# Kernel optimization log

Measured on AMD Instinct MI355X. Metric: run time of the kernel, lower is better.

Reference implementation:

```python
import jax, jax.numpy as jnp
import numpy as np
from jax.ops import segment_sum

N_NODES = 100000
IN, HID, OUT = 512, 128, 40
N_EDGES = 1600000


def gcn_conv(x, W, b, src, dst, n):
    # x: [N, d_in] -> linear transform first (PyG GCNConv applies lin before propagate)
    h = x @ W  # [N, d_out]
    # add self-loops
    loop = jnp.arange(n, dtype=src.dtype)
    s = jnp.concatenate([src, loop])
    d = jnp.concatenate([dst, loop])
    # symmetric normalization deg^{-1/2}[s] * deg^{-1/2}[d], deg over targets incl. self-loops
    deg = segment_sum(jnp.ones_like(d, dtype=h.dtype), d, num_segments=n)
    dinv = jnp.where(deg > 0, jax.lax.rsqrt(deg), 0.0)
    norm = dinv[s] * dinv[d]  # [E+N]
    msg = h[s] * norm[:, None]  # gather + scale
    out = segment_sum(msg, d, num_segments=n)  # scatter-add over edges
    return out + b


def setup_inputs() -> dict:
    key = jax.random.key(0)
    k1, k2, k3, k4, k5, k6 = jax.random.split(key, 6)
    x = jax.random.normal(k1, (N_NODES, IN), dtype=jnp.float32)
    edge_index = jax.random.randint(k2, (2, N_EDGES), 0, N_NODES, dtype=jnp.int64)
    s1 = 1.0 / np.sqrt(IN)
    s2 = 1.0 / np.sqrt(HID)
    W1 = jax.random.uniform(k3, (IN, HID), jnp.float32, -s1, s1)
    b1 = jnp.zeros((HID,), jnp.float32)
    W2 = jax.random.uniform(k4, (HID, OUT), jnp.float32, -s2, s2)
    b2 = jnp.zeros((OUT,), jnp.float32)
    return {"x": x, "edge_index": edge_index, "W1": W1, "b1": b1, "W2": W2, "b2": b2}


def reference(x, edge_index, W1, b1, W2, b2):
    src, dst = edge_index[0], edge_index[1]
    n = x.shape[0]
    # CRD: GCNConv -> relu (dropout is identity in eval mode)
    h = jax.nn.relu(gcn_conv(x, W1, b1, src, dst, n))
    # CLS: GCNConv -> log_softmax
    out = gcn_conv(h, W2, b2, src, dst, n)
    return jax.nn.log_softmax(out, axis=1)
```

## Files before the change

### kernel.cpp

```cpp
#include <hip/hip_runtime.h>
#include <hip/hip_bf16.h>

typedef unsigned short u16;
typedef __attribute__((ext_vector_type(8))) short short8;
typedef __attribute__((ext_vector_type(4))) float f32x4;

#define NN   100000
#define NE   1600000
#define DIN  512
#define DHID 128
#define DOUT 40
#define NB   98

__device__ __forceinline__ float bf2f(u16 u) {
  union { unsigned int i; float f; } v; v.i = ((unsigned int)u) << 16; return v.f;
}
__device__ __forceinline__ u16 f2bf(float f) {
  __hip_bfloat16 h = __float2bfloat16(f);
  return *reinterpret_cast<u16*>(&h);
}


__global__ __launch_bounds__(256) void k_count(const int* __restrict__ ei, int* __restrict__ cnt) {
  int base = (blockIdx.x * 256 + threadIdx.x) * 4;
  if (base >= NE) return;
  int4 d4 = *(const int4*)&ei[NE + base];
  atomicAdd(&cnt[d4.x], 1);
  atomicAdd(&cnt[d4.y], 1);
  atomicAdd(&cnt[d4.z], 1);
  atomicAdd(&cnt[d4.w], 1);
}

__global__ __launch_bounds__(256) void k_dinv(const int* __restrict__ cnt, float* __restrict__ dinv) {
  int i = blockIdx.x * 256 + threadIdx.x;
  if (i < NN) dinv[i] = rsqrtf((float)(cnt[i] + 1));
}

__global__ __launch_bounds__(256) void k_blocksum(const int* __restrict__ cnt, int* __restrict__ bsum) {
  __shared__ int s[256];
  int b = blockIdx.x, t = threadIdx.x;
  int base = b * 1024 + t * 4;
  int tot = 0;
  if (base < NN) { int4 v = *(const int4*)&cnt[base]; tot = v.x + v.y + v.z + v.w; }
  s[t] = tot; __syncthreads();
  for (int o = 128; o > 0; o >>= 1) { if (t < o) s[t] += s[t + o]; __syncthreads(); }
  if (t == 0) bsum[b] = s[0];
}

__global__ __launch_bounds__(128) void k_scanbsum(int* __restrict__ bsum) {
  __shared__ int s[128];
  int t = threadIdx.x;
  int v = (t < NB) ? bsum[t] : 0;
  s[t] = v; __syncthreads();
  for (int o = 1; o < 128; o <<= 1) {
    int add = (t >= o) ? s[t - o] : 0;
    __syncthreads();
    s[t] += add;
    __syncthreads();
  }
  if (t < NB) bsum[t] = s[t] - v;
}

__global__ __launch_bounds__(256) void k_scan3(const int* __restrict__ cnt, const int* __restrict__ bsum,
                                               int* __restrict__ offs, int* __restrict__ cur) {
  __shared__ int s[256];
  int b = blockIdx.x, t = threadIdx.x;
  int base = b * 1024 + t * 4;
  int4 v = make_int4(0, 0, 0, 0);
  if (base < NN) v = *(const int4*)&cnt[base];
  int tot = v.x + v.y + v.z + v.w;
  s[t] = tot; __syncthreads();
  for (int o = 1; o < 256; o <<= 1) {
    int add = (t >= o) ? s[t - o] : 0;
    __syncthreads();
    s[t] += add;
    __syncthreads();
  }
  int tp = s[t] - tot;
  int b0 = bsum[b] + tp;
  if (base < NN) {
    int4 o4;
    o4.x = b0;
    o4.y = b0 + v.x;
    o4.z = b0 + v.x + v.y;
    o4.w = b0 + v.x + v.y + v.z;
    *(int4*)&offs[base] = o4;
    *(int4*)&cur[base]  = o4;
  }
  if (b == 0 && t == 0) offs[NN] = NE;
}

__global__ __launch_bounds__(256) void k_scatter(const int* __restrict__ ei, int* __restrict__ cur,
                                                 const float* __restrict__ dinv, int2* __restrict__ ep) {
  int base = (blockIdx.x * 256 + threadIdx.x) * 4;
  if (base >= NE) return;
  int4 s4 = *(const int4*)&ei[base];
  int4 d4 = *(const int4*)&ei[NE + base];
  int p0 = atomicAdd(&cur[d4.x], 1);
  int p1 = atomicAdd(&cur[d4.y], 1);
  int p2 = atomicAdd(&cur[d4.z], 1);
  int p3 = atomicAdd(&cur[d4.w], 1);
  ep[p0] = make_int2(s4.x, __float_as_int(dinv[s4.x]));
  ep[p1] = make_int2(s4.y, __float_as_int(dinv[s4.y]));
  ep[p2] = make_int2(s4.z, __float_as_int(dinv[s4.z]));
  ep[p3] = make_int2(s4.w, __float_as_int(dinv[s4.w]));
}


__global__ __launch_bounds__(256) void k_prepw(const float* __restrict__ W1, u16* __restrict__ wt) {
  int id = blockIdx.x * 256 + threadIdx.x;
  int k = id & 511, n = id >> 9;
  wt[n * DIN + k] = f2bf(W1[k * DHID + n]);
}


#define G1_LOAD(S, C) do { int k0_ = (C) * 64;                                          \
  _Pragma("unroll") for (int it = 0; it < 4; it++) {                                    \
    int u_ = t + it * 256; int row_ = u_ >> 4, seg_ = u_ & 15; int gr_ = row0 + row_;   \
    xv[S][it] = (gr_ < NN) ? *(const float4*)&x[gr_ * DIN + k0_ + seg_ * 4]             \
                           : make_float4(0.f, 0.f, 0.f, 0.f);                           \
    wv[S][it] = *(const uint4*)&wt[(u_ >> 3) * DIN + k0_ + (u_ & 7) * 8];               \
  } } while (0)

#define G1_WRITE(S) do {                                                                \
  _Pragma("unroll") for (int it = 0; it < 4; it++) {                                    \
    int u_ = t + it * 256; int row_ = u_ >> 4, seg_ = u_ & 15;                          \
    float4 v_ = xv[S][it]; ushort4 o_;                                                  \
    o_.x = f2bf(v_.x); o_.y = f2bf(v_.y); o_.z = f2bf(v_.z); o_.w = f2bf(v_.w);         \
    *(ushort4*)&xs[S][row_][seg_ * 4] = o_;                                             \
    *(uint4*)&ws[S][u_ >> 3][(u_ & 7) * 8] = wv[S][it];                                 \
  } } while (0)

#define G1_MFMA(S) do {                                                                 \
  _Pragma("unroll") for (int s2 = 0; s2 < 2; s2++) {                                    \
    short8 a_ = *(const short8*)&xs[S][mbase + lm][s2 * 32 + lq * 8];                   \
    _Pragma("unroll") for (int nt = 0; nt < 8; nt++) {                                  \
      short8 b_ = *(const short8*)&ws[S][nt * 16 + lm][s2 * 32 + lq * 8];               \
      acc[nt] = __builtin_amdgcn_mfma_f32_16x16x32_bf16(a_, b_, acc[nt], 0, 0, 0);      \
    } } } while (0)

#define G1_BAR() do {                                                                   \
    asm volatile("s_waitcnt lgkmcnt(0)" ::: "memory");                                  \
    __builtin_amdgcn_sched_barrier(0);          \
    __builtin_amdgcn_s_barrier();                                                       \
  } while (0)

__global__ __launch_bounds__(256) void k_gemm1(const float* __restrict__ x, const u16* __restrict__ wt,
                                               u16* __restrict__ h1) {
  __shared__ u16 xs[2][64][72];
  __shared__ u16 ws[2][128][72];
  int t = threadIdx.x;
  int row0 = blockIdx.x * 64;
  int w = t >> 6, l = t & 63;
  int lm = l & 15, lq = l >> 4;
  int mbase = w * 16;
  float4 xv[2][4];
  uint4  wv[2][4];
  f32x4 acc[8];
#pragma unroll
  for (int nt = 0; nt < 8; nt++) acc[nt] = (f32x4){0.f, 0.f, 0.f, 0.f};

  G1_LOAD(0, 0);
  G1_LOAD(1, 1);
  G1_WRITE(0);
  G1_BAR();

#pragma unroll
  for (int c = 0; c < 8; c++) {
    if (c + 2 < 8) {
      if ((c & 1) == 0) G1_LOAD(0, c + 2); else G1_LOAD(1, c + 2);
    }
    if ((c & 1) == 0) G1_MFMA(0); else G1_MFMA(1);
    if (c + 1 < 8) {
      if ((c & 1) == 0) G1_WRITE(1); else G1_WRITE(0);
      G1_BAR();
    }
  }

#pragma unroll
  for (int reg = 0; reg < 4; reg++) {
    int gr = row0 + mbase + lq * 4 + reg;
    if (gr < NN) {
#pragma unroll
      for (int nt = 0; nt < 8; nt++) {
        h1[gr * DHID + nt * 16 + lm] = f2bf(acc[nt][reg]);
      }
    }
  }
}


__global__ __launch_bounds__(256) void k_prop1(const u16* __restrict__ h1, const float* __restrict__ dinv,
                                               const int* __restrict__ offs, const int2* __restrict__ ep,
                                               const float* __restrict__ b1, u16* __restrict__ g) {
  int n = blockIdx.x * 4 + (threadIdx.x >> 6);
  int l = threadIdx.x & 63;
  int qtr = l >> 4, c = l & 15;
  int fb = c * 8;
  float dn = dinv[n];
  float a[8];
#pragma unroll
  for (int j = 0; j < 8; j++) a[j] = 0.f;
  if (qtr == 0) {
    short8 sv = *(const short8*)&h1[n * DHID + fb];
#pragma unroll
    for (int j = 0; j < 8; j++) a[j] = dn * bf2f((u16)sv[j]);
  }
  int e1 = offs[n + 1];
  int q = offs[n] + qtr * 4;
  for (; q + 3 < e1; q += 16) {
    int2 ea = ep[q], eb = ep[q + 1], ec = ep[q + 2], ed = ep[q + 3];
    float wa = __int_as_float(ea.y), wb = __int_as_float(eb.y);
    float wc = __int_as_float(ec.y), wd = __int_as_float(ed.y);
    short8 va = *(const short8*)&h1[ea.x * DHID + fb];
    short8 vb = *(const short8*)&h1[eb.x * DHID + fb];
    short8 vc = *(const short8*)&h1[ec.x * DHID + fb];
    short8 vd = *(const short8*)&h1[ed.x * DHID + fb];
#pragma unroll
    for (int j = 0; j < 8; j++)
      a[j] += wa * bf2f((u16)va[j]) + wb * bf2f((u16)vb[j])
            + wc * bf2f((u16)vc[j]) + wd * bf2f((u16)vd[j]);
  }
  for (; q < e1; q++) {
    int2 ea = ep[q];
    float wa = __int_as_float(ea.y);
    short8 va = *(const short8*)&h1[ea.x * DHID + fb];
#pragma unroll
    for (int j = 0; j < 8; j++) a[j] += wa * bf2f((u16)va[j]);
  }
#pragma unroll
  for (int j = 0; j < 8; j++) {
    a[j] += __shfl_xor(a[j], 16);
    a[j] += __shfl_xor(a[j], 32);
  }
  if (qtr == 0) {
    float4 b0 = *(const float4*)&b1[fb];
    float4 b4 = *(const float4*)&b1[fb + 4];
    float bb[8] = {b0.x, b0.y, b0.z, b0.w, b4.x, b4.y, b4.z, b4.w};
    short8 o;
#pragma unroll
    for (int j = 0; j < 8; j++) o[j] = (short)f2bf(fmaxf(bb[j] + dn * a[j], 0.f));
    *(short8*)&g[n * DHID + fb] = o;
  }
}


__global__ __launch_bounds__(320) void k_gemm2(const u16* __restrict__ g, const float* __restrict__ W2,
                                               u16* __restrict__ h2) {
  __shared__ float w2s[DHID][DOUT];
  __shared__ float gs[8][DHID];
  int t = threadIdx.x;
  int row0 = blockIdx.x * 8;
  for (int idx = t; idx < DHID * DOUT; idx += 320) ((float*)w2s)[idx] = W2[idx];
  for (int idx = t; idx < 8 * DHID; idx += 320) {
    int r = idx >> 7, k = idx & 127;
    int gr = row0 + r;
    ((float*)gs)[idx] = (gr < NN) ? bf2f(g[gr * DHID + k]) : 0.f;
  }
  __syncthreads();
  int r = t / DOUT, c = t % DOUT;
  float acc = 0.f;
#pragma unroll
  for (int k = 0; k < DHID; k += 4) {
    float4 gv = *(const float4*)&gs[r][k];
    acc += gv.x * w2s[k][c] + gv.y * w2s[k + 1][c] + gv.z * w2s[k + 2][c] + gv.w * w2s[k + 3][c];
  }
  int gr = row0 + r;
  if (gr < NN) h2[gr * DOUT + c] = f2bf(acc);
}


__global__ __launch_bounds__(256) void k_prop2(const u16* __restrict__ h2, const float* __restrict__ dinv,
                                               const int* __restrict__ offs, const int2* __restrict__ ep,
                                               const float* __restrict__ b2, float* __restrict__ out) {
  int n = blockIdx.x * 4 + (threadIdx.x >> 6);
  int l = threadIdx.x & 63;
  int grp = l >> 5;
  int c2 = l & 31;
  bool act = c2 < 20;
  int f = c2 * 2;
  float dn = dinv[n];
  float a0 = 0.f, a1 = 0.f;
  if (grp == 0 && act) {
    uint sv = *(const uint*)&h2[n * DOUT + f];
    a0 = dn * bf2f((u16)(sv & 0xffffu));
    a1 = dn * bf2f((u16)(sv >> 16));
  }
  int e1 = offs[n + 1];
  int q = offs[n] + grp * 4;
  for (; q + 3 < e1; q += 8) {
    int2 ea = ep[q], eb = ep[q + 1], ec = ep[q + 2], ed = ep[q + 3];
    uint va = act ? *(const uint*)&h2[ea.x * DOUT + f] : 0u;
    uint vb = act ? *(const uint*)&h2[eb.x * DOUT + f] : 0u;
    uint vc = act ? *(const uint*)&h2[ec.x * DOUT + f] : 0u;
    uint vd = act ? *(const uint*)&h2[ed.x * DOUT + f] : 0u;
    float wa = __int_as_float(ea.y), wb = __int_as_float(eb.y);
    float wc = __int_as_float(ec.y), wd = __int_as_float(ed.y);
    a0 += wa * bf2f((u16)(va & 0xffffu)) + wb * bf2f((u16)(vb & 0xffffu))
        + wc * bf2f((u16)(vc & 0xffffu)) + wd * bf2f((u16)(vd & 0xffffu));
    a1 += wa * bf2f((u16)(va >> 16)) + wb * bf2f((u16)(vb >> 16))
        + wc * bf2f((u16)(vc >> 16)) + wd * bf2f((u16)(vd >> 16));
  }
  for (; q < e1; q++) {
    int2 ea = ep[q];
    uint va = act ? *(const uint*)&h2[ea.x * DOUT + f] : 0u;
    float wa = __int_as_float(ea.y);
    a0 += wa * bf2f((u16)(va & 0xffffu));
    a1 += wa * bf2f((u16)(va >> 16));
  }
  a0 += __shfl_xor(a0, 32);
  a1 += __shfl_xor(a1, 32);
  float l0 = act ? (b2[f]     + dn * a0) : -INFINITY;
  float l1 = act ? (b2[f + 1] + dn * a1) : -INFINITY;
  float mx = fmaxf(l0, l1);
#pragma unroll
  for (int o = 16; o > 0; o >>= 1) mx = fmaxf(mx, __shfl_xor(mx, o));
  float pv = act ? (__expf(l0 - mx) + __expf(l1 - mx)) : 0.f;
#pragma unroll
  for (int o = 16; o > 0; o >>= 1) pv += __shfl_xor(pv, o);
  if (grp == 0 && act) {
    float ls = logf(pv);
    *(float2*)&out[n * DOUT + f] = make_float2(l0 - mx - ls, l1 - mx - ls);
  }
}


extern "C" void kernel_launch(void* const* d_in, const int* in_sizes, int n_in,
                              void* d_out, int out_size, void* d_ws, size_t ws_size,
                              hipStream_t stream) {
  const float* x  = (const float*)d_in[0];
  const int* ei   = (const int*)d_in[1];
  const float* W1 = (const float*)d_in[2];
  const float* b1 = (const float*)d_in[3];
  const float* W2 = (const float*)d_in[4];
  const float* b2 = (const float*)d_in[5];
  float* out      = (float*)d_out;

  char* ws = (char*)d_ws;
  int*   cnt    = (int*)(ws + 0);
  float* dinv   = (float*)(ws + 400000);
  int*   offs   = (int*)(ws + 800000);
  int*   bsum   = (int*)(ws + 1200128);
  int2*  ep     = (int2*)(ws + 1200640);
  int*   cur    = (int*)(ws + 14000640);
  u16*   h1     = (u16*)(ws + 20400640);
  u16*   h2     = (u16*)(ws + 20400640);
  u16*   g      = (u16*)(ws + 46000640);
  u16*   wt     = (u16*)(ws + 71600640);

  hipMemsetAsync(cnt, 0, 400000, stream);

  k_count   <<<(NE / 4 + 255) / 256, 256, 0, stream>>>(ei, cnt);
  k_dinv    <<<(NN + 255) / 256, 256, 0, stream>>>(cnt, dinv);
  k_blocksum<<<NB, 256, 0, stream>>>(cnt, bsum);
  k_scanbsum<<<1, 128, 0, stream>>>(bsum);
  k_scan3   <<<NB, 256, 0, stream>>>(cnt, bsum, offs, cur);
  k_scatter <<<(NE / 4 + 255) / 256, 256, 0, stream>>>(ei, cur, dinv, ep);

  k_prepw   <<<(DIN * DHID) / 256, 256, 0, stream>>>(W1, wt);
  k_gemm1   <<<(NN + 63) / 64, 256, 0, stream>>>(x, wt, h1);
  k_prop1   <<<NN / 4, 256, 0, stream>>>(h1, dinv, offs, ep, b1, g);
  k_gemm2   <<<(NN + 7) / 8, 320, 0, stream>>>(g, W2, h2);
  k_prop2   <<<NN / 4, 256, 0, stream>>>(h2, dinv, offs, ep, b2, out);
}
```

Baseline: 734.0 us.

## Retile gemm1 to 128-row blocks with 32-wide K chunks and XOR-swizzled LDS

```diff
diff --git a/kernel.cpp b/kernel.cpp
--- a/kernel.cpp
+++ b/kernel.cpp
@@ -114,30 +114,36 @@
 }
 
 
-#define G1_LOAD(S, C) do { int k0_ = (C) * 64;                                          \
-  _Pragma("unroll") for (int it = 0; it < 4; it++) {                                    \
-    int u_ = t + it * 256; int row_ = u_ >> 4, seg_ = u_ & 15; int gr_ = row0 + row_;   \
-    xv[S][it] = (gr_ < NN) ? *(const float4*)&x[gr_ * DIN + k0_ + seg_ * 4]             \
+#define G1_LOAD(S, C) do { int k0_ = (C) * 32;                                          \
+  _Pragma("unroll") for (int it = 0; it < 2; it++) {                                    \
+    int u_ = t + it * 512; int row_ = u_ >> 3, pc_ = u_ & 7; int gr_ = row0 + row_;     \
+    xv[S][it] = (gr_ < NN) ? *(const float4*)&x[gr_ * DIN + k0_ + pc_ * 4]              \
                            : make_float4(0.f, 0.f, 0.f, 0.f);                           \
-    wv[S][it] = *(const uint4*)&wt[(u_ >> 3) * DIN + k0_ + (u_ & 7) * 8];               \
-  } } while (0)
+  }                                                                                     \
+  wv[S] = *(const uint4*)&wt[(t >> 2) * DIN + k0_ + (t & 3) * 8];                       \
+  } while (0)
 
 #define G1_WRITE(S) do {                                                                \
-  _Pragma("unroll") for (int it = 0; it < 4; it++) {                                    \
-    int u_ = t + it * 256; int row_ = u_ >> 4, seg_ = u_ & 15;                          \
+  _Pragma("unroll") for (int it = 0; it < 2; it++) {                                    \
+    int u_ = t + it * 512; int row_ = u_ >> 3, pc_ = u_ & 7;                            \
+    int sg_ = pc_ >> 1, hf_ = pc_ & 1;                                                  \
+    int sw_ = sg_ ^ ((row_ >> 1) & 3);                                                  \
     float4 v_ = xv[S][it]; ushort4 o_;                                                  \
     o_.x = f2bf(v_.x); o_.y = f2bf(v_.y); o_.z = f2bf(v_.z); o_.w = f2bf(v_.w);         \
-    *(ushort4*)&xs[S][row_][seg_ * 4] = o_;                                             \
-    *(uint4*)&ws[S][u_ >> 3][(u_ & 7) * 8] = wv[S][it];                                 \
+    *(ushort4*)&xs[S][row_][sw_ * 8 + hf_ * 4] = o_;                                    \
+  }                                                                                     \
+  { int n_ = t >> 2, sg_ = t & 3; int sw_ = sg_ ^ ((n_ >> 1) & 3);                      \
+    *(uint4*)&ws[S][n_][sw_ * 8] = wv[S]; }                                             \
+  } while (0)
+
+#define G1_MFMA(S) do {                                                                 \
+  int ar_ = mbase + lm;                                                                 \
+  short8 a_ = *(const short8*)&xs[S][ar_][(lq ^ ((ar_ >> 1) & 3)) * 8];                 \
+  _Pragma("unroll") for (int nt = 0; nt < 8; nt++) {                                    \
+    int br_ = nt * 16 + lm;                                                             \
+    short8 b_ = *(const short8*)&ws[S][br_][(lq ^ ((br_ >> 1) & 3)) * 8];               \
+    acc[nt] = __builtin_amdgcn_mfma_f32_16x16x32_bf16(a_, b_, acc[nt], 0, 0, 0);        \
   } } while (0)
-
-#define G1_MFMA(S) do {                                                                 \
-  _Pragma("unroll") for (int s2 = 0; s2 < 2; s2++) {                                    \
-    short8 a_ = *(const short8*)&xs[S][mbase + lm][s2 * 32 + lq * 8];                   \
-    _Pragma("unroll") for (int nt = 0; nt < 8; nt++) {                                  \
-      short8 b_ = *(const short8*)&ws[S][nt * 16 + lm][s2 * 32 + lq * 8];               \
-      acc[nt] = __builtin_amdgcn_mfma_f32_16x16x32_bf16(a_, b_, acc[nt], 0, 0, 0);      \
-    } } } while (0)
 
 #define G1_BAR() do {                                                                   \
     asm volatile("s_waitcnt lgkmcnt(0)" ::: "memory");                                  \
@@ -145,17 +151,17 @@
     __builtin_amdgcn_s_barrier();                                                       \
   } while (0)
 
-__global__ __launch_bounds__(256) void k_gemm1(const float* __restrict__ x, const u16* __restrict__ wt,
-                                               u16* __restrict__ h1) {
-  __shared__ u16 xs[2][64][72];
-  __shared__ u16 ws[2][128][72];
+__global__ __launch_bounds__(512, 4) void k_gemm1(const float* __restrict__ x, const u16* __restrict__ wt,
+                                                  u16* __restrict__ h1) {
+  __shared__ u16 xs[2][128][32];
+  __shared__ u16 ws[2][128][32];
   int t = threadIdx.x;
-  int row0 = blockIdx.x * 64;
+  int row0 = blockIdx.x * 128;
   int w = t >> 6, l = t & 63;
   int lm = l & 15, lq = l >> 4;
   int mbase = w * 16;
-  float4 xv[2][4];
-  uint4  wv[2][4];
+  float4 xv[2][2];
+  uint4  wv[2];
   f32x4 acc[8];
 #pragma unroll
   for (int nt = 0; nt < 8; nt++) acc[nt] = (f32x4){0.f, 0.f, 0.f, 0.f};
@@ -166,12 +172,12 @@
   G1_BAR();
 
 #pragma unroll
-  for (int c = 0; c < 8; c++) {
-    if (c + 2 < 8) {
+  for (int c = 0; c < 16; c++) {
+    if (c + 2 < 16) {
       if ((c & 1) == 0) G1_LOAD(0, c + 2); else G1_LOAD(1, c + 2);
     }
     if ((c & 1) == 0) G1_MFMA(0); else G1_MFMA(1);
-    if (c + 1 < 8) {
+    if (c + 1 < 16) {
       if ((c & 1) == 0) G1_WRITE(1); else G1_WRITE(0);
       G1_BAR();
     }
@@ -358,7 +364,7 @@
   k_scatter <<<(NE / 4 + 255) / 256, 256, 0, stream>>>(ei, cur, dinv, ep);
 
   k_prepw   <<<(DIN * DHID) / 256, 256, 0, stream>>>(W1, wt);
-  k_gemm1   <<<(NN + 63) / 64, 256, 0, stream>>>(x, wt, h1);
+  k_gemm1   <<<(NN + 127) / 128, 512, 0, stream>>>(x, wt, h1);
   k_prop1   <<<NN / 4, 256, 0, stream>>>(h1, dinv, offs, ep, b1, g);
   k_gemm2   <<<(NN + 7) / 8, 320, 0, stream>>>(g, W2, h2);
   k_prop2   <<<NN / 4, 256, 0, stream>>>(h2, dinv, offs, ep, b2, out);
```

Result: faster. 707.9 us (-3.6%).
